# Kernel optimization log

Measured on AMD Instinct MI355X. Metric: run time of the kernel, lower is better.

The kernel has to match this reference:

```python
import jax, jax.numpy as jnp
import numpy as np

N_NODES = 50000
N_EDGES = 640000
IN_FEAT = 128
OUT_FEAT = 128


def setup_inputs() -> dict:
    key = jax.random.key(0)
    k1, k2, k3 = jax.random.split(key, 3)
    features = jax.random.normal(k1, (N_NODES, IN_FEAT), dtype=jnp.float32)
    edges = jax.random.randint(k2, (2, N_EDGES), 0, N_NODES, dtype=jnp.int64)
    # glorot_uniform for [in_feat, out_feat]
    limit = np.sqrt(6.0 / (IN_FEAT + OUT_FEAT)).astype(np.float32)
    weight = jax.random.uniform(k3, (IN_FEAT, OUT_FEAT), dtype=jnp.float32,
                                minval=-limit, maxval=limit)
    return {"features": features, "edges": edges, "weight": weight}


def reference(features, edges, weight):
    num_nodes = features.shape[0]
    # self representation: [N, out_feat]
    nodes_representation = features @ weight
    # gather source-node features per edge: [E, in_feat]
    neighbour_representations = features[edges[1]]
    # unsorted_segment_mean over destination ids (empty segments -> 0)
    summed = jax.ops.segment_sum(neighbour_representations, edges[0],
                                 num_segments=num_nodes)
    counts = jax.ops.segment_sum(jnp.ones((edges.shape[1],), jnp.float32),
                                 edges[0], num_segments=num_nodes)
    aggregated = jnp.where(counts[:, None] > 0,
                           summed / jnp.maximum(counts, 1.0)[:, None], 0.0)
    aggregated_messages = aggregated @ weight  # [N, out_feat]
    return jax.nn.relu(jnp.concatenate([nodes_representation,
                                        aggregated_messages], axis=-1))
```

## Files before the change

### kernel.cpp

```cpp
#include <hip/hip_runtime.h>

#define N_NODES 50000
#define N_EDGES 640000
#define IN_FEAT 128
#define OUT_FEAT 128
#define CAP 48
#define NBINS 49
#define NBLK 625
#define CAP2 56
#define NSLICE2 32
#define NPART 16
#define CAP3 64
#define GEMM_BLOCKS 1250
#define FUSED_BLOCKS 1875

typedef unsigned int u32;
typedef unsigned short u16t;
typedef __attribute__((ext_vector_type(8))) short bf16x8;
typedef __attribute__((ext_vector_type(4))) float f32x4;

__device__ __forceinline__ u16t f2bf(float f) {
    union { float f; u32 u; } v; v.f = f;
    u32 r = (v.u + 0x7fffu + ((v.u >> 16) & 1u)) >> 16;
    return (u16t)r;
}
__device__ __forceinline__ float blo(u32 p) {
    union { u32 u; float f; } v; v.u = p << 16; return v.f;
}
__device__ __forceinline__ float bhi(u32 p) {
    union { u32 u; float f; } v; v.u = p & 0xffff0000u; return v.f;
}

__global__ __launch_bounds__(256) void k_fused(const float* __restrict__ feats,
                                               const float* __restrict__ weight,
                                               const int* __restrict__ edges,
                                               u16t* __restrict__ Ybf,
                                               float* __restrict__ out,
                                               int* __restrict__ cnt1,
                                               u32* __restrict__ binbufD) {
    __shared__ float T[16][132];
    __shared__ int cur[64];
    int tid = threadIdx.x;
    int role3 = blockIdx.x % 3;
    if (role3 == 0) {
        int blk = blockIdx.x / 3;
        int e0 = (blk * 256 + tid) * 4;
        int4 d4 = *reinterpret_cast<const int4*>(edges + e0);
        int4 s4 = *reinterpret_cast<const int4*>(edges + N_EDGES + e0);
        if (tid < 64) cur[tid] = 0;
        __syncthreads();
        int b0 = d4.x >> 10, b1 = d4.y >> 10, b2 = d4.z >> 10, b3 = d4.w >> 10;
        int o0 = atomicAdd(&cur[b0], 1);
        if (o0 < CAP2) binbufD[(size_t)(b0 * NBLK + blk) * CAP2 + o0] =
            ((u32)(d4.x & 1023) << 16) | (u32)s4.x;
        int o1 = atomicAdd(&cur[b1], 1);
        if (o1 < CAP2) binbufD[(size_t)(b1 * NBLK + blk) * CAP2 + o1] =
            ((u32)(d4.y & 1023) << 16) | (u32)s4.y;
        int o2 = atomicAdd(&cur[b2], 1);
        if (o2 < CAP2) binbufD[(size_t)(b2 * NBLK + blk) * CAP2 + o2] =
            ((u32)(d4.z & 1023) << 16) | (u32)s4.z;
        int o3 = atomicAdd(&cur[b3], 1);
        if (o3 < CAP2) binbufD[(size_t)(b3 * NBLK + blk) * CAP2 + o3] =
            ((u32)(d4.w & 1023) << 16) | (u32)s4.w;
        __syncthreads();
        if (tid < NBINS) {
            int c = cur[tid];
            cnt1[tid * NBLK + blk] = (c < CAP2) ? c : CAP2;
        }
        return;
    }
    int gemm_id = (blockIdx.x / 3) * 2 + role3 - 1;
    int wid = tid >> 6, lane = tid & 63;
    int ncol0 = wid * 32;
    int krow = lane >> 4;
    int nl = lane & 15;
    int tr = tid >> 4;
    int tc = (tid & 15) * 8;
    bf16x8 bfrag[4][2];
    #pragma unroll
    for (int kb = 0; kb < 4; ++kb) {
        #pragma unroll
        for (int nt = 0; nt < 2; ++nt) {
            bf16x8 b;
            #pragma unroll
            for (int j = 0; j < 8; ++j) {
                int k = kb * 32 + krow * 8 + j;
                b[j] = (short)f2bf(weight[(size_t)k * OUT_FEAT + ncol0 + nt * 16 + nl]);
            }
            bfrag[kb][nt] = b;
        }
    }
    for (int mt = gemm_id; mt < N_NODES / 16; mt += GEMM_BLOCKS) {
        const float* arow = feats + (size_t)(mt * 16 + nl) * IN_FEAT + krow * 8;
        f32x4 acc0 = {0.f, 0.f, 0.f, 0.f};
        f32x4 acc1 = {0.f, 0.f, 0.f, 0.f};
        #pragma unroll
        for (int kb = 0; kb < 4; ++kb) {
            float4 a0 = *reinterpret_cast<const float4*>(arow + kb * 32);
            float4 a1 = *reinterpret_cast<const float4*>(arow + kb * 32 + 4);
            bf16x8 a;
            a[0] = (short)f2bf(a0.x); a[1] = (short)f2bf(a0.y);
            a[2] = (short)f2bf(a0.z); a[3] = (short)f2bf(a0.w);
            a[4] = (short)f2bf(a1.x); a[5] = (short)f2bf(a1.y);
            a[6] = (short)f2bf(a1.z); a[7] = (short)f2bf(a1.w);
            acc0 = __builtin_amdgcn_mfma_f32_16x16x32_bf16(a, bfrag[kb][0], acc0, 0, 0, 0);
            acc1 = __builtin_amdgcn_mfma_f32_16x16x32_bf16(a, bfrag[kb][1], acc1, 0, 0, 0);
        }
        __syncthreads();
        #pragma unroll
        for (int r = 0; r < 4; ++r) {
            T[krow * 4 + r][ncol0 + nl]      = acc0[r];
            T[krow * 4 + r][ncol0 + 16 + nl] = acc1[r];
        }
        __syncthreads();
        int node = mt * 16 + tr;
        float4 v0 = *reinterpret_cast<const float4*>(&T[tr][tc]);
        float4 v1 = *reinterpret_cast<const float4*>(&T[tr][tc + 4]);
        bf16x8 yb;
        yb[0] = (short)f2bf(v0.x); yb[1] = (short)f2bf(v0.y);
        yb[2] = (short)f2bf(v0.z); yb[3] = (short)f2bf(v0.w);
        yb[4] = (short)f2bf(v1.x); yb[5] = (short)f2bf(v1.y);
        yb[6] = (short)f2bf(v1.z); yb[7] = (short)f2bf(v1.w);
        *reinterpret_cast<bf16x8*>(Ybf + (size_t)node * OUT_FEAT + tc) = yb;
        float4 r0, r1;
        r0.x = fmaxf(v0.x, 0.f); r0.y = fmaxf(v0.y, 0.f);
        r0.z = fmaxf(v0.z, 0.f); r0.w = fmaxf(v0.w, 0.f);
        r1.x = fmaxf(v1.x, 0.f); r1.y = fmaxf(v1.y, 0.f);
        r1.z = fmaxf(v1.z, 0.f); r1.w = fmaxf(v1.w, 0.f);
        float* orow = out + (size_t)node * (2 * OUT_FEAT) + tc;
        *reinterpret_cast<float4*>(orow)     = r0;
        *reinterpret_cast<float4*>(orow + 4) = r1;
    }
}

__global__ __launch_bounds__(256) void k_shuf(const int* __restrict__ cnt1,
                                              const u32* __restrict__ binbufD,
                                              int* __restrict__ cnt2,
                                              u32* __restrict__ binbuf2) {
    __shared__ int cur2[NSLICE2];
    int tid = threadIdx.x;
    int bin = blockIdx.x >> 4, part = blockIdx.x & 15;
    if (tid < NSLICE2) cur2[tid] = 0;
    __syncthreads();
    int s = (NBLK * part) >> 4, e = (NBLK * (part + 1)) >> 4;
    for (int blk = s + (tid >> 4); blk < e; blk += 16) {
        int n = cnt1[bin * NBLK + blk];
        const u32* seg = binbufD + (size_t)(bin * NBLK + blk) * CAP2;
        for (int j = tid & 15; j < n; j += 16) {
            u32 p = seg[j];
            int sl = (int)((p >> 21) & 31u);
            int o = atomicAdd(&cur2[sl], 1);
            if (o < CAP3)
                binbuf2[(size_t)((bin * NSLICE2 + sl) * NPART + part) * CAP3 + o] = p;
        }
    }
    __syncthreads();
    if (tid < NSLICE2) {
        int c = cur2[tid];
        cnt2[(bin * NSLICE2 + tid) * NPART + part] = (c < CAP3) ? c : CAP3;
    }
}

__global__ __launch_bounds__(256) void k_acc(const u16t* __restrict__ Ybf,
                                             const int* __restrict__ cnt2,
                                             const u32* __restrict__ binbuf2,
                                             float* __restrict__ out) {
    __shared__ u16t lbkt[NSLICE2 * CAP];
    __shared__ int lcnt[NSLICE2];
    int tid = threadIdx.x;
    int bin = blockIdx.x >> 5, slice = blockIdx.x & 31;
    if (tid < NSLICE2) lcnt[tid] = 0;
    __syncthreads();
    int base2 = (bin * NSLICE2 + slice) * NPART;
    {
        int p = tid >> 4;
        int n = cnt2[base2 + p];
        const u32* seg = binbuf2 + (size_t)(base2 + p) * CAP3;
        for (int j = tid & 15; j < n; j += 16) {
            u32 pk = seg[j];
            int da = (int)((pk >> 16) & 31u);
            int pos = atomicAdd(&lcnt[da], 1);
            if (pos < CAP) lbkt[da * CAP + pos] = (u16t)(pk & 0xffffu);
        }
    }
    __syncthreads();
    int wid = tid >> 6, lane = tid & 63;
    int half = lane >> 5, l5 = lane & 31;
    for (int i = 0; i < 8; ++i) {
        int r = wid * 8 + i;
        int node = (bin << 10) + (slice << 5) + r;
        if (node >= N_NODES) break;
        int deg = lcnt[r];
        int m = (deg < CAP) ? deg : CAP;
        const u16t* b = &lbkt[r * CAP];
        float s0 = 0.f, s1 = 0.f, s2 = 0.f, s3 = 0.f;
        int j = half;
        for (; j + 7 <= m; j += 8) {
            int sa = (int)b[j], sb = (int)b[j + 2], sc = (int)b[j + 4], sd = (int)b[j + 6];
            uint2 pa = *reinterpret_cast<const uint2*>(Ybf + (size_t)sa * OUT_FEAT + 4 * l5);
            uint2 pb = *reinterpret_cast<const uint2*>(Ybf + (size_t)sb * OUT_FEAT + 4 * l5);
            uint2 pc = *reinterpret_cast<const uint2*>(Ybf + (size_t)sc * OUT_FEAT + 4 * l5);
            uint2 pd = *reinterpret_cast<const uint2*>(Ybf + (size_t)sd * OUT_FEAT + 4 * l5);
            s0 += (blo(pa.x) + blo(pb.x)) + (blo(pc.x) + blo(pd.x));
            s1 += (bhi(pa.x) + bhi(pb.x)) + (bhi(pc.x) + bhi(pd.x));
            s2 += (blo(pa.y) + blo(pb.y)) + (blo(pc.y) + blo(pd.y));
            s3 += (bhi(pa.y) + bhi(pb.y)) + (bhi(pc.y) + bhi(pd.y));
        }
        for (; j < m; j += 2) {
            int sa = (int)b[j];
            uint2 pa = *reinterpret_cast<const uint2*>(Ybf + (size_t)sa * OUT_FEAT + 4 * l5);
            s0 += blo(pa.x); s1 += bhi(pa.x);
            s2 += blo(pa.y); s3 += bhi(pa.y);
        }
        s0 += __shfl_xor(s0, 32); s1 += __shfl_xor(s1, 32);
        s2 += __shfl_xor(s2, 32); s3 += __shfl_xor(s3, 32);
        if (half == 0) {
            float inv = (deg > 0) ? 1.f / (float)deg : 0.f;
            float4 v;
            v.x = fmaxf(s0 * inv, 0.f); v.y = fmaxf(s1 * inv, 0.f);
            v.z = fmaxf(s2 * inv, 0.f); v.w = fmaxf(s3 * inv, 0.f);
            *reinterpret_cast<float4*>(out + (size_t)node * (2 * OUT_FEAT) + OUT_FEAT + 4 * l5) = v;
        }
    }
}

extern "C" void kernel_launch(void* const* d_in, const int* in_sizes, int n_in,
                              void* d_out, int out_size, void* d_ws, size_t ws_size,
                              hipStream_t stream) {
    const float* feats  = (const float*)d_in[0];
    const int*   edges  = (const int*)d_in[1];
    const float* weight = (const float*)d_in[2];
    float* out = (float*)d_out;

    u16t* Ybf     = (u16t*)d_ws;
    int*  cnt1    = (int*)(Ybf + (size_t)N_NODES * OUT_FEAT);
    u32*  binbufD = (u32*)(cnt1 + NBINS * NBLK);
    int*  cnt2    = (int*)(binbufD + (size_t)NBINS * NBLK * CAP2);
    u32*  binbuf2 = (u32*)(cnt2 + NBINS * NSLICE2 * NPART);

    hipLaunchKernelGGL(k_fused, dim3(FUSED_BLOCKS), dim3(256), 0, stream,
                       feats, weight, edges, Ybf, out, cnt1, binbufD);
    hipLaunchKernelGGL(k_shuf,  dim3(NBINS * NPART), dim3(256), 0, stream,
                       cnt1, binbufD, cnt2, binbuf2);
    hipLaunchKernelGGL(k_acc,   dim3(NBINS * NSLICE2), dim3(256), 0, stream,
                       Ybf, cnt2, binbuf2, out);
}
```

Measured before the change: 61.79 us.

## Write GEMM outputs directly from MFMA registers and rebalance fused block roles

Removes the shared-memory transpose stage, along with its two barriers, that turned MFMA accumulators into row-contiguous vector stores. Each lane now writes scalar bf16 and fp32 values straight from its accumulator registers. The fused kernel also changes from a 1:2 bin-to-GEMM block ratio to 1:1, halving the number of GEMM blocks so each does more tiles. The direct writes are narrower and less coalesced (2-byte and 4-byte stores strided across rows), which may increase memory transactions in exchange for dropping the LDS traffic and syncs.

```diff
diff --git a/kernel.cpp b/kernel.cpp
--- a/kernel.cpp
+++ b/kernel.cpp
@@ -11,8 +11,8 @@
 #define NSLICE2 32
 #define NPART 16
 #define CAP3 64
-#define GEMM_BLOCKS 1250
-#define FUSED_BLOCKS 1875
+#define GEMM_BLOCKS 625
+#define FUSED_BLOCKS 1250
 
 typedef unsigned int u32;
 typedef unsigned short u16t;
@@ -38,12 +38,10 @@
                                                float* __restrict__ out,
                                                int* __restrict__ cnt1,
                                                u32* __restrict__ binbufD) {
-    __shared__ float T[16][132];
     __shared__ int cur[64];
     int tid = threadIdx.x;
-    int role3 = blockIdx.x % 3;
-    if (role3 == 0) {
-        int blk = blockIdx.x / 3;
+    if (blockIdx.x & 1) {
+        int blk = blockIdx.x >> 1;
         int e0 = (blk * 256 + tid) * 4;
         int4 d4 = *reinterpret_cast<const int4*>(edges + e0);
         int4 s4 = *reinterpret_cast<const int4*>(edges + N_EDGES + e0);
@@ -69,13 +67,11 @@
         }
         return;
     }
-    int gemm_id = (blockIdx.x / 3) * 2 + role3 - 1;
+    int gemm_id = blockIdx.x >> 1;
     int wid = tid >> 6, lane = tid & 63;
     int ncol0 = wid * 32;
     int krow = lane >> 4;
     int nl = lane & 15;
-    int tr = tid >> 4;
-    int tc = (tid & 15) * 8;
     bf16x8 bfrag[4][2];
     #pragma unroll
     for (int kb = 0; kb < 4; ++kb) {
@@ -106,30 +102,16 @@
             acc0 = __builtin_amdgcn_mfma_f32_16x16x32_bf16(a, bfrag[kb][0], acc0, 0, 0, 0);
             acc1 = __builtin_amdgcn_mfma_f32_16x16x32_bf16(a, bfrag[kb][1], acc1, 0, 0, 0);
         }
-        __syncthreads();
         #pragma unroll
         for (int r = 0; r < 4; ++r) {
-            T[krow * 4 + r][ncol0 + nl]      = acc0[r];
-            T[krow * 4 + r][ncol0 + 16 + nl] = acc1[r];
-        }
-        __syncthreads();
-        int node = mt * 16 + tr;
-        float4 v0 = *reinterpret_cast<const float4*>(&T[tr][tc]);
-        float4 v1 = *reinterpret_cast<const float4*>(&T[tr][tc + 4]);
-        bf16x8 yb;
-        yb[0] = (short)f2bf(v0.x); yb[1] = (short)f2bf(v0.y);
-        yb[2] = (short)f2bf(v0.z); yb[3] = (short)f2bf(v0.w);
-        yb[4] = (short)f2bf(v1.x); yb[5] = (short)f2bf(v1.y);
-        yb[6] = (short)f2bf(v1.z); yb[7] = (short)f2bf(v1.w);
-        *reinterpret_cast<bf16x8*>(Ybf + (size_t)node * OUT_FEAT + tc) = yb;
-        float4 r0, r1;
-        r0.x = fmaxf(v0.x, 0.f); r0.y = fmaxf(v0.y, 0.f);
-        r0.z = fmaxf(v0.z, 0.f); r0.w = fmaxf(v0.w, 0.f);
-        r1.x = fmaxf(v1.x, 0.f); r1.y = fmaxf(v1.y, 0.f);
-        r1.z = fmaxf(v1.z, 0.f); r1.w = fmaxf(v1.w, 0.f);
-        float* orow = out + (size_t)node * (2 * OUT_FEAT) + tc;
-        *reinterpret_cast<float4*>(orow)     = r0;
-        *reinterpret_cast<float4*>(orow + 4) = r1;
+            int node = mt * 16 + krow * 4 + r;
+            int c0 = ncol0 + nl, c1 = ncol0 + 16 + nl;
+            float v0 = acc0[r], v1 = acc1[r];
+            Ybf[(size_t)node * OUT_FEAT + c0] = f2bf(v0);
+            Ybf[(size_t)node * OUT_FEAT + c1] = f2bf(v1);
+            out[(size_t)node * (2 * OUT_FEAT) + c0] = fmaxf(v0, 0.f);
+            out[(size_t)node * (2 * OUT_FEAT) + c1] = fmaxf(v1, 0.f);
+        }
     }
 }
 
```

After: 70.15 us. +13.5%, slower.
